# Kernel optimization log

Measured on AMD Instinct MI355X. Metric: run time of the kernel, lower is better.

Reference implementation:

```python
import jax, jax.numpy as jnp
import numpy as np

HEADS = 16
DIM_HEAD = 64
SCALE = DIM_HEAD ** -0.5
EPS = 1e-5


def _bitlinear(x, w):
    """BitNet b1.58 BitLinear (kyegomez/BitNet), eval-mode, bias-free.
    w: [out, in] torch-layout. Ternary weight quant (scale = mean|w|),
    per-token int8 absmax activation quant, straight-through estimator.
    """
    ws = 1.0 / jnp.clip(jnp.mean(jnp.abs(w)), EPS, None)
    wq = jnp.clip(jnp.round(w * ws), -1.0, 1.0) / ws
    wq = w + jax.lax.stop_gradient(wq - w)
    xs = 127.0 / jnp.clip(jnp.max(jnp.abs(x), axis=-1, keepdims=True), EPS, None)
    xq = jnp.clip(jnp.round(x * xs), -128.0, 127.0) / xs
    xq = x + jax.lax.stop_gradient(xq - x)
    return jnp.einsum('bnd,od->bno', xq, wq)


def setup_inputs() -> dict:
    key = jax.random.key(0)
    ks = jax.random.split(key, 6)
    b, n, d = 2, 2048, 1024
    return {
        'x': jax.random.normal(ks[0], (b, n, d), dtype=jnp.float32),
        'context': jax.random.normal(ks[1], (b, n, d), dtype=jnp.float32),
        'Wq': jax.random.normal(ks[2], (d, d), dtype=jnp.float32) * 0.02,
        'Wk': jax.random.normal(ks[3], (d, d), dtype=jnp.float32) * 0.02,
        'Wv': jax.random.normal(ks[4], (d, d), dtype=jnp.float32) * 0.02,
        'Wo': jax.random.normal(ks[5], (d, d), dtype=jnp.float32) * 0.02,
    }


def reference(x, context, Wq, Wk, Wv, Wo):
    b, n, _ = x.shape
    m = context.shape[1]
    q = _bitlinear(x, Wq)
    k = _bitlinear(context, Wk)
    v = _bitlinear(context, Wv)
    # b n (h d) -> b h n d
    q = q.reshape(b, n, HEADS, DIM_HEAD).transpose(0, 2, 1, 3)
    k = k.reshape(b, m, HEADS, DIM_HEAD).transpose(0, 2, 1, 3)
    v = v.reshape(b, m, HEADS, DIM_HEAD).transpose(0, 2, 1, 3)
    dots = jnp.einsum('bhid,bhjd->bhij', q, k) * SCALE
    attn = jax.nn.softmax(dots, axis=-1)  # dropout is identity in eval
    out = jnp.einsum('bhij,bhjd->bhid', attn, v)
    out = out.transpose(0, 2, 1, 3).reshape(b, n, HEADS * DIM_HEAD)
    return _bitlinear(out, Wo)
```

## Files before the change

### kernel.cpp

```cpp
#include <hip/hip_runtime.h>
#include <math.h>

#define HEADS   16
#define DHEAD   64
#define SEQ     2048
#define NB      2
#define DM      1024
#define NTOK    4096
#define WEPS    1e-5

using f16x8   = __attribute__((ext_vector_type(8))) _Float16;
using f16x4   = __attribute__((ext_vector_type(4))) _Float16;
using floatx4 = __attribute__((ext_vector_type(4))) float;
using i32x4   = __attribute__((ext_vector_type(4))) int;

typedef __attribute__((address_space(1))) unsigned int gu32;
typedef __attribute__((address_space(3))) unsigned int lu32;

#define BAR_LGKM()  asm volatile("s_waitcnt lgkmcnt(0)\n\ts_barrier" ::: "memory")
#define WAIT_LGKM() asm volatile("s_waitcnt lgkmcnt(0)" ::: "memory")

__device__ __forceinline__ unsigned pack2(_Float16 a, _Float16 b) {
    union { _Float16 h[2]; unsigned u; } c; c.h[0] = a; c.h[1] = b; return c.u;
}
__device__ __forceinline__ _Float16 lo16(unsigned u) {
    union { unsigned u; _Float16 h[2]; } c; c.u = u; return c.h[0];
}
__device__ __forceinline__ _Float16 hi16(unsigned u) {
    union { unsigned u; _Float16 h[2]; } c; c.u = u; return c.h[1];
}
__device__ __forceinline__ unsigned short h16b(_Float16 h) {
    union { _Float16 h; unsigned short u; } c; c.h = h; return c.u;
}

__global__ void wsum1(const float* __restrict__ w0, const float* __restrict__ w1,
                      const float* __restrict__ w2, const float* __restrict__ w3,
                      double* __restrict__ partial) {
    const float* w = (blockIdx.y == 0) ? w0 : (blockIdx.y == 1) ? w1 : (blockIdx.y == 2) ? w2 : w3;
    int base = blockIdx.x * 16384;
    double s = 0.0;
    for (int i = threadIdx.x; i < 16384; i += 256)
        s += fabs((double)w[base + i]);
    __shared__ double sd[256];
    sd[threadIdx.x] = s;
    __syncthreads();
    for (int st = 128; st > 0; st >>= 1) {
        if (threadIdx.x < st) sd[threadIdx.x] += sd[threadIdx.x + st];
        __syncthreads();
    }
    if (threadIdx.x == 0) partial[blockIdx.y * 64 + blockIdx.x] = sd[0];
}

__global__ void wsum2(const double* __restrict__ partial, double* __restrict__ wscale) {
    int t = threadIdx.x;
    if (t < 4) {
        double s = 0.0;
        for (int i = 0; i < 64; i++) s += partial[t * 64 + i];
        double mean = s / (1024.0 * 1024.0);
        wscale[t] = (mean > WEPS) ? mean : WEPS;
    }
}

__global__ void wquant(const float* __restrict__ w0, const float* __restrict__ w1,
                       const float* __restrict__ w2, const float* __restrict__ w3,
                       const double* __restrict__ wscale, signed char* __restrict__ wq) {
    int widx = blockIdx.y;
    const float* w = (widx == 0) ? w0 : (widx == 1) ? w1 : (widx == 2) ? w2 : w3;
    double ws = 1.0 / wscale[widx];
    int idx = (blockIdx.x * 256 + threadIdx.x) * 4;
    float4 wv = *(const float4*)(w + idx);
    char4 o;
    {
        double r = rint((double)wv.x * ws); r = r > 1.0 ? 1.0 : (r < -1.0 ? -1.0 : r); o.x = (signed char)r;
    } {
        double r = rint((double)wv.y * ws); r = r > 1.0 ? 1.0 : (r < -1.0 ? -1.0 : r); o.y = (signed char)r;
    } {
        double r = rint((double)wv.z * ws); r = r > 1.0 ? 1.0 : (r < -1.0 ? -1.0 : r); o.z = (signed char)r;
    } {
        double r = rint((double)wv.w * ws); r = r > 1.0 ? 1.0 : (r < -1.0 ? -1.0 : r); o.w = (signed char)r;
    }
    *(char4*)(wq + (size_t)widx * 1048576 + idx) = o;
}

__device__ __forceinline__ void aquant_row(const float* __restrict__ row,
                                           signed char* __restrict__ dst_row,
                                           double* __restrict__ ascale_p) {
    int t = threadIdx.x;
    float4 xv = *(const float4*)(row + t * 4);
    float a = fmaxf(fmaxf(fabsf(xv.x), fabsf(xv.y)), fmaxf(fabsf(xv.z), fabsf(xv.w)));
    __shared__ float sm[256];
    sm[t] = a;
    __syncthreads();
    for (int st = 128; st > 0; st >>= 1) {
        if (t < st) sm[t] = fmaxf(sm[t], sm[t + st]);
        __syncthreads();
    }
    double mx = (double)sm[0];
    if (mx < WEPS) mx = WEPS;
    if (t == 0) *ascale_p = mx / 127.0;
    double xs = 127.0 / mx;
    char4 o;
    {
        double r = rint((double)xv.x * xs); r = r > 127.0 ? 127.0 : (r < -128.0 ? -128.0 : r); o.x = (signed char)r;
    } {
        double r = rint((double)xv.y * xs); r = r > 127.0 ? 127.0 : (r < -128.0 ? -128.0 : r); o.y = (signed char)r;
    } {
        double r = rint((double)xv.z * xs); r = r > 127.0 ? 127.0 : (r < -128.0 ? -128.0 : r); o.z = (signed char)r;
    } {
        double r = rint((double)xv.w * xs); r = r > 127.0 ? 127.0 : (r < -128.0 ? -128.0 : r); o.w = (signed char)r;
    }
    *(char4*)(dst_row + t * 4) = o;
}

__global__ void aquant(const float* __restrict__ src, signed char* __restrict__ dst,
                       double* __restrict__ ascale) {
    int tok = blockIdx.x;
    aquant_row(src + (size_t)tok * DM, dst + (size_t)tok * DM, ascale + tok);
}

__global__ void aquant2(const float* __restrict__ x, const float* __restrict__ ctx,
                        signed char* __restrict__ dst, double* __restrict__ ascale) {
    int tok = blockIdx.x;
    const float* row = (tok < NTOK) ? x + (size_t)tok * DM : ctx + (size_t)(tok - NTOK) * DM;
    aquant_row(row, dst + (size_t)tok * DM, ascale + tok);
}

__device__ __forceinline__ void gemm_core(
        const signed char* __restrict__ A, const signed char* __restrict__ W,
        const double* __restrict__ ascale, double wsc,
        void* __restrict__ outp, int mode, float prescale, int bx, int by) {
    __shared__ __align__(16) signed char lds_a[128 * 64];
    __shared__ __align__(16) signed char lds_b[128 * 64];
    const int tid  = threadIdx.x;
    const int wave = tid >> 6, lane = tid & 63;
    const int wr = wave >> 1, wc = wave & 1;
    const int quad = lane >> 4, l15 = lane & 15;
    const int row0 = by * 128, col0 = bx * 128;
    i32x4 acc[4][4] = {};

    const signed char* ga0 = A + (size_t)(row0 + (lane >> 2)) * DM + (lane & 3) * 16;
    const signed char* gb0 = W + (size_t)(col0 + (lane >> 2)) * DM + (lane & 3) * 16;

    for (int k0 = 0; k0 < DM; k0 += 64) {
        __syncthreads();
        #pragma unroll
        for (int t = 0; t < 2; t++) {
            const int i = wave + t * 4;
            __builtin_amdgcn_global_load_lds(
                (const gu32*)(const void*)(ga0 + (size_t)i * 16 * DM + k0),
                (lu32*)(void*)(lds_a + i * 1024), 16, 0, 0);
            __builtin_amdgcn_global_load_lds(
                (const gu32*)(const void*)(gb0 + (size_t)i * 16 * DM + k0),
                (lu32*)(void*)(lds_b + i * 1024), 16, 0, 0);
        }
        __syncthreads();
        i32x4 af[4], bfr[4];
        #pragma unroll
        for (int mi = 0; mi < 4; mi++) {
            int r = wr * 64 + mi * 16 + l15;
            af[mi] = *(const i32x4*)&lds_a[r * 64 + quad * 16];
        }
        #pragma unroll
        for (int ni = 0; ni < 4; ni++) {
            int n = wc * 64 + ni * 16 + l15;
            bfr[ni] = *(const i32x4*)&lds_b[n * 64 + quad * 16];
        }
        #pragma unroll
        for (int mi = 0; mi < 4; mi++)
            #pragma unroll
            for (int ni = 0; ni < 4; ni++)
                acc[mi][ni] = __builtin_amdgcn_mfma_i32_16x16x64_i8(af[mi], bfr[ni], acc[mi][ni], 0, 0, 0);
    }

    #pragma unroll
    for (int mi = 0; mi < 4; mi++) {
        int tbase = row0 + wr * 64 + mi * 16 + quad * 4;
        #pragma unroll
        for (int reg = 0; reg < 4; reg++) {
            int t = tbase + reg;
            double sa = ascale[t] * wsc;
            #pragma unroll
            for (int ni = 0; ni < 4; ni++) {
                int o = col0 + wc * 64 + ni * 16 + l15;
                float val = (float)((double)acc[mi][ni][reg] * sa);
                if (mode == 1) {
                    ((float*)outp)[(size_t)t * DM + o] = val;
                } else {
                    int bb = t >> 11, n = t & 2047, hh = o >> 6, dh = o & 63;
                    float fv = val * prescale;
                    _Float16 hl = (_Float16)fv;
                    _Float16 ml = (_Float16)((fv - (float)hl) * 2048.0f);
                    if (mode == 0) {
                        size_t idx = (((size_t)(bb * HEADS + hh) * SEQ + n) << 6) + dh;
                        ((unsigned short*)outp)[idx]           = h16b(hl);
                        ((unsigned short*)outp)[idx + 4194304] = h16b(ml);
                    } else {
                        ((unsigned*)outp)[(((size_t)(bb * HEADS + hh) * 64 + dh) << 11) + n] = pack2(hl, ml);
                    }
                }
            }
        }
    }
}

__global__ __launch_bounds__(256) void gemm_qkv(
        const signed char* __restrict__ xq, const signed char* __restrict__ cq,
        const signed char* __restrict__ wqb, const double* __restrict__ ascale_x,
        const double* __restrict__ wscale, void* __restrict__ qkv) {
    const int which = blockIdx.x >> 3;
    char* base = (char*)qkv + (size_t)which * 16777216;
    gemm_core(which == 0 ? xq : cq,
              wqb + (size_t)which * 1048576,
              ascale_x + (which ? NTOK : 0),
              wscale[which],
              base,
              which == 2 ? 2 : 0,
              which == 0 ? 0.18033688011112042f : 1.0f, blockIdx.x & 7, blockIdx.y);
}

__global__ __launch_bounds__(256) void gemm_o(
        const signed char* __restrict__ aq, const signed char* __restrict__ wo,
        const double* __restrict__ ascale, const double* __restrict__ wscale_p,
        float* __restrict__ out) {
    gemm_core(aq, wo, ascale, *wscale_p, out, 1, 1.0f, blockIdx.x, blockIdx.y);
}

#define KH_IDX(row, d8) (((row) * 8 + ((d8) ^ ((row) & 7))) * 8)

__global__ __launch_bounds__(256, 2) void attn_mfma(
        const unsigned short* __restrict__ qhg, const unsigned short* __restrict__ qlg,
        const unsigned short* __restrict__ khg, const unsigned short* __restrict__ klg,
        const unsigned* __restrict__ vg, float* __restrict__ out) {
    __shared__ __align__(16) _Float16 KhL[32 * 64];
    __shared__ __align__(16) _Float16 KlL[32 * 64];
    __shared__ __align__(16) _Float16 PhL[4][32 * 36];
    __shared__ __align__(16) _Float16 PlL[4][32 * 36];
    __shared__ float Lp[4][2][16][4];

    const int lin  = blockIdx.x;
    const int bh   = (lin & 7) * 4 + (lin >> 7);
    const int qblk = (lin >> 3) & 15;
    const int tid  = threadIdx.x;
    const int wave = tid >> 6, lane = tid & 63;
    const int l15  = lane & 15, quad = lane >> 4;
    const int qbase = qblk * 128 + wave * 32;

    f16x8 qh[2][2], qm[2][2];
    #pragma unroll
    for (int qs = 0; qs < 2; qs++) {
        #pragma unroll
        for (int c = 0; c < 2; c++) {
            size_t off = (((size_t)bh * SEQ + qbase + qs * 16 + l15) << 6) + c * 32 + quad * 8;
            qh[qs][c] = *(const f16x8*)(qhg + off);
            qm[qs][c] = *(const f16x8*)(qlg + off);
        }
    }

    floatx4 och[2][4] = {};
    floatx4 ocm[2][4] = {};
    float lsum[2] = {0.f, 0.f};

    const unsigned short* khb = khg + ((size_t)bh * SEQ << 6);
    const unsigned short* klb = klg + ((size_t)bh * SEQ << 6);
    const unsigned* vbase = vg + ((size_t)bh << 17);

    const int kk = tid >> 3, d8 = tid & 7;

    uint4 kh_pf = *(const uint4*)(khb + ((size_t)kk << 6) + d8 * 8);
    uint4 kl_pf = *(const uint4*)(klb + ((size_t)kk << 6) + d8 * 8);

    for (int kt = 0; kt < SEQ; kt += 32) {
        uint4 va[4], vb[4];
        #pragma unroll
        for (int nh = 0; nh < 4; nh++) {
            const unsigned* vp = vbase + (((size_t)(nh * 16 + l15)) << 11) + kt + quad * 8;
            va[nh] = *(const uint4*)vp;
            vb[nh] = *(const uint4*)(vp + 4);
        }

        BAR_LGKM();

        *(uint4*)&KhL[KH_IDX(kk, d8)] = kh_pf;
        *(uint4*)&KlL[KH_IDX(kk, d8)] = kl_pf;

        if (kt + 32 < SEQ) {
            kh_pf = *(const uint4*)(khb + ((size_t)(kt + 32 + kk) << 6) + d8 * 8);
            kl_pf = *(const uint4*)(klb + ((size_t)(kt + 32 + kk) << 6) + d8 * 8);
        }

        BAR_LGKM();

        f16x8 kfh[2][2], kfl[2][2];
        #pragma unroll
        for (int ms = 0; ms < 2; ms++) {
            #pragma unroll
            for (int c = 0; c < 2; c++) {
                kfh[ms][c] = *(const f16x8*)&KhL[KH_IDX(ms * 16 + l15, c * 4 + quad)];
                kfl[ms][c] = *(const f16x8*)&KlL[KH_IDX(ms * 16 + l15, c * 4 + quad)];
            }
        }

        #pragma unroll
        for (int qs = 0; qs < 2; qs++) {
            #pragma unroll
            for (int ms = 0; ms < 2; ms++) {
                floatx4 ah = {}, am = {};
                #pragma unroll
                for (int c = 0; c < 2; c++) {
                    ah = __builtin_amdgcn_mfma_f32_16x16x32_f16(kfh[ms][c], qh[qs][c], ah, 0, 0, 0);
                    am = __builtin_amdgcn_mfma_f32_16x16x32_f16(kfh[ms][c], qm[qs][c], am, 0, 0, 0);
                    am = __builtin_amdgcn_mfma_f32_16x16x32_f16(kfl[ms][c], qh[qs][c], am, 0, 0, 0);
                }
                float p[4];
                #pragma unroll
                for (int r = 0; r < 4; r++) {
                    float s = ah[r] + am[r] * 4.8828125e-4f;
                    p[r] = exp2f(s);
                    lsum[qs] += p[r];
                }
                f16x4 hv, lv;
                #pragma unroll
                for (int r = 0; r < 4; r++) {
                    _Float16 h = (_Float16)p[r];
                    hv[r] = h;
                    lv[r] = (_Float16)((p[r] - (float)h) * 2048.0f);
                }
                int poff = (qs * 16 + l15) * 36 + ms * 16 + quad * 4;
                *(f16x4*)&PhL[wave][poff] = hv;
                *(f16x4*)&PlL[wave][poff] = lv;
            }
        }
        WAIT_LGKM();

        f16x8 vfh[4], vfm[4];
        #pragma unroll
        for (int nh = 0; nh < 4; nh++) {
            unsigned wd[8] = {va[nh].x, va[nh].y, va[nh].z, va[nh].w,
                              vb[nh].x, vb[nh].y, vb[nh].z, vb[nh].w};
            #pragma unroll
            for (int j = 0; j < 8; j++) { vfh[nh][j] = lo16(wd[j]); vfm[nh][j] = hi16(wd[j]); }
        }
        #pragma unroll
        for (int qs = 0; qs < 2; qs++) {
            f16x8 pfh = *(const f16x8*)&PhL[wave][(qs * 16 + l15) * 36 + quad * 8];
            f16x8 pfm = *(const f16x8*)&PlL[wave][(qs * 16 + l15) * 36 + quad * 8];
            #pragma unroll
            for (int nh = 0; nh < 4; nh++) {
                och[qs][nh] = __builtin_amdgcn_mfma_f32_16x16x32_f16(pfh, vfh[nh], och[qs][nh], 0, 0, 0);
                ocm[qs][nh] = __builtin_amdgcn_mfma_f32_16x16x32_f16(pfh, vfm[nh], ocm[qs][nh], 0, 0, 0);
                ocm[qs][nh] = __builtin_amdgcn_mfma_f32_16x16x32_f16(pfm, vfh[nh], ocm[qs][nh], 0, 0, 0);
            }
        }
    }

    Lp[wave][0][l15][quad] = lsum[0];
    Lp[wave][1][l15][quad] = lsum[1];
    WAIT_LGKM();

    int b = bh >> 4, h = bh & 15;
    #pragma unroll
    for (int qs = 0; qs < 2; qs++) {
        float linv[4];
        #pragma unroll
        for (int r = 0; r < 4; r++) {
            float4 lv = *(const float4*)&Lp[wave][qs][quad * 4 + r][0];
            linv[r] = 1.0f / (lv.x + lv.y + lv.z + lv.w);
        }
        #pragma unroll
        for (int nh = 0; nh < 4; nh++) {
            #pragma unroll
            for (int r = 0; r < 4; r++) {
                int token = b * SEQ + qbase + qs * 16 + quad * 4 + r;
                float val = (och[qs][nh][r] + ocm[qs][nh][r] * 4.8828125e-4f) * linv[r];
                out[(size_t)token * DM + h * 64 + nh * 16 + l15] = val;
            }
        }
    }
}

extern "C" void kernel_launch(void* const* d_in, const int* in_sizes, int n_in,
                              void* d_out, int out_size, void* d_ws, size_t ws_size,
                              hipStream_t stream) {
    const float* x       = (const float*)d_in[0];
    const float* context = (const float*)d_in[1];
    const float* Wq      = (const float*)d_in[2];
    const float* Wk      = (const float*)d_in[3];
    const float* Wv      = (const float*)d_in[4];
    const float* Wo      = (const float*)d_in[5];
    char* ws = (char*)d_ws;

    double* wscale   = (double*)(ws + 0);
    double* partial  = (double*)(ws + 4096);
    double* ascale_x = (double*)(ws + 8192);
    double* ascale_a = (double*)(ws + 73728);
    signed char* wqb = (signed char*)(ws + 131072);
    signed char* xq  = (signed char*)(ws + 4325376);
    signed char* cq  = (signed char*)(ws + 8519680);
    float* attn_out  = (float*)(ws + 4325376);
    char* planes     = ws + 21102592;
    signed char* aq  = (signed char*)(ws + 21102592);

    unsigned short* qhg = (unsigned short*)planes;
    unsigned short* qlg = qhg + 4194304;
    unsigned short* khg = (unsigned short*)(planes + 16777216);
    unsigned short* klg = khg + 4194304;
    unsigned*       vpg = (unsigned*)(planes + 33554432);

    wsum1<<<dim3(64, 4), 256, 0, stream>>>(Wq, Wk, Wv, Wo, partial);
    wsum2<<<1, 64, 0, stream>>>(partial, wscale);
    wquant<<<dim3(1024, 4), 256, 0, stream>>>(Wq, Wk, Wv, Wo, wscale, wqb);
    aquant2<<<2 * NTOK, 256, 0, stream>>>(x, context, xq, ascale_x);

    gemm_qkv<<<dim3(24, 32), 256, 0, stream>>>(xq, cq, wqb, ascale_x, wscale, planes);

    attn_mfma<<<dim3(512), 256, 0, stream>>>(qhg, qlg, khg, klg, vpg, attn_out);

    aquant<<<NTOK, 256, 0, stream>>>(attn_out, aq, ascale_a);
    gemm_o<<<dim3(8, 32), 256, 0, stream>>>(aq, wqb + 3145728, ascale_a, wscale + 3, (float*)d_out);
}
```

Measured before the change: 300.2 us.

## Stage V tiles in shared memory and halve per-block query tile in attention

The attention kernel now gives each wave 16 query rows instead of 32 and launches twice as many blocks, targeting higher occupancy (launch bounds raised to 4 blocks). V tiles are no longer loaded straight from global memory into registers by every wave. They are now cooperatively prefetched, split into high and low fp16 planes, and stored in swizzled shared memory that all waves read from. This is meant to cut redundant global V traffic and register pressure. The cost is more K/V tile loading per query row, since each block now covers fewer queries, plus extra LDS writes and reads.

```diff
diff --git a/kernel.cpp b/kernel.cpp
--- a/kernel.cpp
+++ b/kernel.cpp
@@ -227,65 +227,79 @@
 
 #define KH_IDX(row, d8) (((row) * 8 + ((d8) ^ ((row) & 7))) * 8)
 
-__global__ __launch_bounds__(256, 2) void attn_mfma(
+__global__ __launch_bounds__(256, 4) void attn_mfma(
         const unsigned short* __restrict__ qhg, const unsigned short* __restrict__ qlg,
         const unsigned short* __restrict__ khg, const unsigned short* __restrict__ klg,
         const unsigned* __restrict__ vg, float* __restrict__ out) {
     __shared__ __align__(16) _Float16 KhL[32 * 64];
     __shared__ __align__(16) _Float16 KlL[32 * 64];
-    __shared__ __align__(16) _Float16 PhL[4][32 * 36];
-    __shared__ __align__(16) _Float16 PlL[4][32 * 36];
-    __shared__ float Lp[4][2][16][4];
+    __shared__ __align__(16) _Float16 VhL[64 * 32];
+    __shared__ __align__(16) _Float16 VlL[64 * 32];
+    __shared__ __align__(16) _Float16 PhL[4][16 * 36];
+    __shared__ __align__(16) _Float16 PlL[4][16 * 36];
+    __shared__ float Lp[4][16][4];
 
     const int lin  = blockIdx.x;
-    const int bh   = (lin & 7) * 4 + (lin >> 7);
-    const int qblk = (lin >> 3) & 15;
+    const int bh   = (lin & 7) * 4 + (lin >> 8);
+    const int qblk = (lin >> 3) & 31;
     const int tid  = threadIdx.x;
     const int wave = tid >> 6, lane = tid & 63;
     const int l15  = lane & 15, quad = lane >> 4;
-    const int qbase = qblk * 128 + wave * 32;
-
-    f16x8 qh[2][2], qm[2][2];
+    const int qbase = qblk * 64 + wave * 16;
+
+    f16x8 qh[2], qm[2];
     #pragma unroll
-    for (int qs = 0; qs < 2; qs++) {
-        #pragma unroll
-        for (int c = 0; c < 2; c++) {
-            size_t off = (((size_t)bh * SEQ + qbase + qs * 16 + l15) << 6) + c * 32 + quad * 8;
-            qh[qs][c] = *(const f16x8*)(qhg + off);
-            qm[qs][c] = *(const f16x8*)(qlg + off);
-        }
-    }
-
-    floatx4 och[2][4] = {};
-    floatx4 ocm[2][4] = {};
-    float lsum[2] = {0.f, 0.f};
+    for (int c = 0; c < 2; c++) {
+        size_t off = (((size_t)bh * SEQ + qbase + l15) << 6) + c * 32 + quad * 8;
+        qh[c] = *(const f16x8*)(qhg + off);
+        qm[c] = *(const f16x8*)(qlg + off);
+    }
+
+    floatx4 och[4] = {};
+    floatx4 ocm[4] = {};
+    float lsum = 0.f;
 
     const unsigned short* khb = khg + ((size_t)bh * SEQ << 6);
     const unsigned short* klb = klg + ((size_t)bh * SEQ << 6);
     const unsigned* vbase = vg + ((size_t)bh << 17);
 
     const int kk = tid >> 3, d8 = tid & 7;
+    const int vrow = tid >> 2, vc = tid & 3;
+    const int vcs  = vc ^ (vrow & 3);
+    const unsigned* vsrc = vbase + ((size_t)vrow << 11) + vc * 8;
 
     uint4 kh_pf = *(const uint4*)(khb + ((size_t)kk << 6) + d8 * 8);
     uint4 kl_pf = *(const uint4*)(klb + ((size_t)kk << 6) + d8 * 8);
+    uint4 vp0 = *(const uint4*)(vsrc);
+    uint4 vp1 = *(const uint4*)(vsrc + 4);
 
     for (int kt = 0; kt < SEQ; kt += 32) {
-        uint4 va[4], vb[4];
-        #pragma unroll
-        for (int nh = 0; nh < 4; nh++) {
-            const unsigned* vp = vbase + (((size_t)(nh * 16 + l15)) << 11) + kt + quad * 8;
-            va[nh] = *(const uint4*)vp;
-            vb[nh] = *(const uint4*)(vp + 4);
-        }
-
         BAR_LGKM();
 
         *(uint4*)&KhL[KH_IDX(kk, d8)] = kh_pf;
         *(uint4*)&KlL[KH_IDX(kk, d8)] = kl_pf;
+
+        uint4 vh4, vl4;
+        {
+            unsigned w0 = vp0.x, w1 = vp0.y, w2 = vp0.z, w3 = vp0.w;
+            vh4.x = (w0 & 0xffffu) | (w1 << 16);
+            vl4.x = (w0 >> 16)     | (w1 & 0xffff0000u);
+            vh4.y = (w2 & 0xffffu) | (w3 << 16);
+            vl4.y = (w2 >> 16)     | (w3 & 0xffff0000u);
+            w0 = vp1.x; w1 = vp1.y; w2 = vp1.z; w3 = vp1.w;
+            vh4.z = (w0 & 0xffffu) | (w1 << 16);
+            vl4.z = (w0 >> 16)     | (w1 & 0xffff0000u);
+            vh4.w = (w0 = vp1.z, (w0 & 0xffffu)) | (vp1.w << 16);
+            vl4.w = (vp1.z >> 16)  | (vp1.w & 0xffff0000u);
+        }
+        *(uint4*)&VhL[(vrow * 4 + vcs) * 8] = vh4;
+        *(uint4*)&VlL[(vrow * 4 + vcs) * 8] = vl4;
 
         if (kt + 32 < SEQ) {
             kh_pf = *(const uint4*)(khb + ((size_t)(kt + 32 + kk) << 6) + d8 * 8);
             kl_pf = *(const uint4*)(klb + ((size_t)(kt + 32 + kk) << 6) + d8 * 8);
+            vp0 = *(const uint4*)(vsrc + kt + 32);
+            vp1 = *(const uint4*)(vsrc + kt + 36);
         }
 
         BAR_LGKM();
@@ -301,79 +315,65 @@
         }
 
         #pragma unroll
-        for (int qs = 0; qs < 2; qs++) {
-            #pragma unroll
-            for (int ms = 0; ms < 2; ms++) {
-                floatx4 ah = {}, am = {};
-                #pragma unroll
-                for (int c = 0; c < 2; c++) {
-                    ah = __builtin_amdgcn_mfma_f32_16x16x32_f16(kfh[ms][c], qh[qs][c], ah, 0, 0, 0);
-                    am = __builtin_amdgcn_mfma_f32_16x16x32_f16(kfh[ms][c], qm[qs][c], am, 0, 0, 0);
-                    am = __builtin_amdgcn_mfma_f32_16x16x32_f16(kfl[ms][c], qh[qs][c], am, 0, 0, 0);
-                }
-                float p[4];
-                #pragma unroll
-                for (int r = 0; r < 4; r++) {
-                    float s = ah[r] + am[r] * 4.8828125e-4f;
-                    p[r] = exp2f(s);
-                    lsum[qs] += p[r];
-                }
-                f16x4 hv, lv;
-                #pragma unroll
-                for (int r = 0; r < 4; r++) {
-                    _Float16 h = (_Float16)p[r];
-                    hv[r] = h;
-                    lv[r] = (_Float16)((p[r] - (float)h) * 2048.0f);
-                }
-                int poff = (qs * 16 + l15) * 36 + ms * 16 + quad * 4;
-                *(f16x4*)&PhL[wave][poff] = hv;
-                *(f16x4*)&PlL[wave][poff] = lv;
+        for (int ms = 0; ms < 2; ms++) {
+            floatx4 ah = {}, am = {};
+            #pragma unroll
+            for (int c = 0; c < 2; c++) {
+                ah = __builtin_amdgcn_mfma_f32_16x16x32_f16(kfh[ms][c], qh[c], ah, 0, 0, 0);
+                am = __builtin_amdgcn_mfma_f32_16x16x32_f16(kfh[ms][c], qm[c], am, 0, 0, 0);
+                am = __builtin_amdgcn_mfma_f32_16x16x32_f16(kfl[ms][c], qh[c], am, 0, 0, 0);
             }
+            float p[4];
+            #pragma unroll
+            for (int r = 0; r < 4; r++) {
+                float s = ah[r] + am[r] * 4.8828125e-4f;
+                p[r] = exp2f(s);
+                lsum += p[r];
+            }
+            f16x4 hv, lv;
+            #pragma unroll
+            for (int r = 0; r < 4; r++) {
+                _Float16 h = (_Float16)p[r];
+                hv[r] = h;
+                lv[r] = (_Float16)((p[r] - (float)h) * 2048.0f);
+            }
+            int poff = l15 * 36 + ms * 16 + quad * 4;
+            *(f16x4*)&PhL[wave][poff] = hv;
+            *(f16x4*)&PlL[wave][poff] = lv;
         }
         WAIT_LGKM();
 
-        f16x8 vfh[4], vfm[4];
+        f16x8 pfh = *(const f16x8*)&PhL[wave][l15 * 36 + quad * 8];
+        f16x8 pfm = *(const f16x8*)&PlL[wave][l15 * 36 + quad * 8];
         #pragma unroll
         for (int nh = 0; nh < 4; nh++) {
-            unsigned wd[8] = {va[nh].x, va[nh].y, va[nh].z, va[nh].w,
-                              vb[nh].x, vb[nh].y, vb[nh].z, vb[nh].w};
-            #pragma unroll
-            for (int j = 0; j < 8; j++) { vfh[nh][j] = lo16(wd[j]); vfm[nh][j] = hi16(wd[j]); }
-        }
-        #pragma unroll
-        for (int qs = 0; qs < 2; qs++) {
-            f16x8 pfh = *(const f16x8*)&PhL[wave][(qs * 16 + l15) * 36 + quad * 8];
-            f16x8 pfm = *(const f16x8*)&PlL[wave][(qs * 16 + l15) * 36 + quad * 8];
-            #pragma unroll
-            for (int nh = 0; nh < 4; nh++) {
-                och[qs][nh] = __builtin_amdgcn_mfma_f32_16x16x32_f16(pfh, vfh[nh], och[qs][nh], 0, 0, 0);
-                ocm[qs][nh] = __builtin_amdgcn_mfma_f32_16x16x32_f16(pfh, vfm[nh], ocm[qs][nh], 0, 0, 0);
-                ocm[qs][nh] = __builtin_amdgcn_mfma_f32_16x16x32_f16(pfm, vfh[nh], ocm[qs][nh], 0, 0, 0);
-            }
-        }
-    }
-
-    Lp[wave][0][l15][quad] = lsum[0];
-    Lp[wave][1][l15][quad] = lsum[1];
+            int vro = nh * 16 + l15;
+            int vof = (vro * 4 + (quad ^ (vro & 3))) * 8;
+            f16x8 vfh = *(const f16x8*)&VhL[vof];
+            f16x8 vfm = *(const f16x8*)&VlL[vof];
+            och[nh] = __builtin_amdgcn_mfma_f32_16x16x32_f16(pfh, vfh, och[nh], 0, 0, 0);
+            ocm[nh] = __builtin_amdgcn_mfma_f32_16x16x32_f16(pfh, vfm, ocm[nh], 0, 0, 0);
+            ocm[nh] = __builtin_amdgcn_mfma_f32_16x16x32_f16(pfm, vfh, ocm[nh], 0, 0, 0);
+        }
+    }
+
+    Lp[wave][l15][quad] = lsum;
     WAIT_LGKM();
 
     int b = bh >> 4, h = bh & 15;
+    float linv[4];
     #pragma unroll
-    for (int qs = 0; qs < 2; qs++) {
-        float linv[4];
+    for (int r = 0; r < 4; r++) {
+        float4 lv = *(const float4*)&Lp[wave][quad * 4 + r][0];
+        linv[r] = 1.0f / (lv.x + lv.y + lv.z + lv.w);
+    }
+    #pragma unroll
+    for (int nh = 0; nh < 4; nh++) {
         #pragma unroll
         for (int r = 0; r < 4; r++) {
-            float4 lv = *(const float4*)&Lp[wave][qs][quad * 4 + r][0];
-            linv[r] = 1.0f / (lv.x + lv.y + lv.z + lv.w);
-        }
-        #pragma unroll
-        for (int nh = 0; nh < 4; nh++) {
-            #pragma unroll
-            for (int r = 0; r < 4; r++) {
-                int token = b * SEQ + qbase + qs * 16 + quad * 4 + r;
-                float val = (och[qs][nh][r] + ocm[qs][nh][r] * 4.8828125e-4f) * linv[r];
-                out[(size_t)token * DM + h * 64 + nh * 16 + l15] = val;
-            }
+            int token = b * SEQ + qbase + quad * 4 + r;
+            float val = (och[nh][r] + ocm[nh][r] * 4.8828125e-4f) * linv[r];
+            out[(size_t)token * DM + h * 64 + nh * 16 + l15] = val;
         }
     }
 }
@@ -413,7 +413,7 @@
 
     gemm_qkv<<<dim3(24, 32), 256, 0, stream>>>(xq, cq, wqb, ascale_x, wscale, planes);
 
-    attn_mfma<<<dim3(512), 256, 0, stream>>>(qhg, qlg, khg, klg, vpg, attn_out);
+    attn_mfma<<<dim3(1024), 256, 0, stream>>>(qhg, qlg, khg, klg, vpg, attn_out);
 
     aquant<<<NTOK, 256, 0, stream>>>(attn_out, aq, ascale_a);
     gemm_o<<<dim3(8, 32), 256, 0, stream>>>(aq, wqb + 3145728, ascale_a, wscale + 3, (float*)d_out);
```

New measurement: 304.4 us. About the same (+1.4%).

## Tile V into separate hi/lo planes per 32-key block and restructure attention loop

Applied to the files above, without the earlier changes.

The V projection epilogue now writes separate fp16 hi and lo planes in a tiled [bh][key tile][dh][32] layout with vectorized 4-element stores, replacing the packed interleaved u32 layout. This lets the attention kernel load V fragments directly without unpacking, and it prefetches the next tile's V after the PV MFMAs. The attention loop also separates the QK MFMAs from the softmax, wraps the MFMA sections in s_setprio, uses hardware exp2 and packed RTZ conversion, and remaps the block-to-(bh, qblk) ordering. RTZ conversion changes rounding slightly, and register pressure rises from holding the prefetched V fragments.

```diff
diff --git a/kernel.cpp b/kernel.cpp
--- a/kernel.cpp
+++ b/kernel.cpp
@@ -11,6 +11,7 @@
 
 using f16x8   = __attribute__((ext_vector_type(8))) _Float16;
 using f16x4   = __attribute__((ext_vector_type(4))) _Float16;
+using fp16x2  = __attribute__((ext_vector_type(2))) __fp16;
 using floatx4 = __attribute__((ext_vector_type(4))) float;
 using i32x4   = __attribute__((ext_vector_type(4))) int;
 
@@ -20,17 +21,11 @@
 #define BAR_LGKM()  asm volatile("s_waitcnt lgkmcnt(0)\n\ts_barrier" ::: "memory")
 #define WAIT_LGKM() asm volatile("s_waitcnt lgkmcnt(0)" ::: "memory")
 
-__device__ __forceinline__ unsigned pack2(_Float16 a, _Float16 b) {
-    union { _Float16 h[2]; unsigned u; } c; c.h[0] = a; c.h[1] = b; return c.u;
-}
-__device__ __forceinline__ _Float16 lo16(unsigned u) {
-    union { unsigned u; _Float16 h[2]; } c; c.u = u; return c.h[0];
-}
-__device__ __forceinline__ _Float16 hi16(unsigned u) {
-    union { unsigned u; _Float16 h[2]; } c; c.u = u; return c.h[1];
-}
 __device__ __forceinline__ unsigned short h16b(_Float16 h) {
     union { _Float16 h; unsigned short u; } c; c.h = h; return c.u;
+}
+__device__ __forceinline__ unsigned pk2u(fp16x2 v) {
+    union { fp16x2 h; unsigned u; } c; c.h = v; return c.u;
 }
 
 __global__ void wsum1(const float* __restrict__ w0, const float* __restrict__ w1,
@@ -175,27 +170,46 @@
     #pragma unroll
     for (int mi = 0; mi < 4; mi++) {
         int tbase = row0 + wr * 64 + mi * 16 + quad * 4;
-        #pragma unroll
-        for (int reg = 0; reg < 4; reg++) {
-            int t = tbase + reg;
-            double sa = ascale[t] * wsc;
+        if (mode == 2) {
+            int bb = tbase >> 11, n = tbase & 2047;
+            int tile = n >> 5, tin = n & 31;
             #pragma unroll
             for (int ni = 0; ni < 4; ni++) {
                 int o = col0 + wc * 64 + ni * 16 + l15;
-                float val = (float)((double)acc[mi][ni][reg] * sa);
-                if (mode == 1) {
-                    ((float*)outp)[(size_t)t * DM + o] = val;
-                } else {
-                    int bb = t >> 11, n = t & 2047, hh = o >> 6, dh = o & 63;
-                    float fv = val * prescale;
+                int hh = o >> 6, dh = o & 63;
+                ushort4 hv, lv;
+                #pragma unroll
+                for (int reg = 0; reg < 4; reg++) {
+                    double sa = ascale[tbase + reg] * wsc;
+                    float fv = (float)((double)acc[mi][ni][reg] * sa) * prescale;
                     _Float16 hl = (_Float16)fv;
                     _Float16 ml = (_Float16)((fv - (float)hl) * 2048.0f);
-                    if (mode == 0) {
+                    ((unsigned short*)&hv)[reg] = h16b(hl);
+                    ((unsigned short*)&lv)[reg] = h16b(ml);
+                }
+                size_t idx = (((size_t)(bb * HEADS + hh) * 64 + tile) * 64 + dh) * 32 + tin;
+                *(ushort4*)((unsigned short*)outp + idx)           = hv;
+                *(ushort4*)((unsigned short*)outp + idx + 4194304) = lv;
+            }
+        } else {
+            #pragma unroll
+            for (int reg = 0; reg < 4; reg++) {
+                int t = tbase + reg;
+                double sa = ascale[t] * wsc;
+                #pragma unroll
+                for (int ni = 0; ni < 4; ni++) {
+                    int o = col0 + wc * 64 + ni * 16 + l15;
+                    float val = (float)((double)acc[mi][ni][reg] * sa);
+                    if (mode == 1) {
+                        ((float*)outp)[(size_t)t * DM + o] = val;
+                    } else {
+                        int bb = t >> 11, n = t & 2047, hh = o >> 6, dh = o & 63;
+                        float fv = val * prescale;
+                        _Float16 hl = (_Float16)fv;
+                        _Float16 ml = (_Float16)((fv - (float)hl) * 2048.0f);
                         size_t idx = (((size_t)(bb * HEADS + hh) * SEQ + n) << 6) + dh;
                         ((unsigned short*)outp)[idx]           = h16b(hl);
                         ((unsigned short*)outp)[idx + 4194304] = h16b(ml);
-                    } else {
-                        ((unsigned*)outp)[(((size_t)(bb * HEADS + hh) * 64 + dh) << 11) + n] = pack2(hl, ml);
                     }
                 }
             }
@@ -230,7 +244,8 @@
 __global__ __launch_bounds__(256, 2) void attn_mfma(
         const unsigned short* __restrict__ qhg, const unsigned short* __restrict__ qlg,
         const unsigned short* __restrict__ khg, const unsigned short* __restrict__ klg,
-        const unsigned* __restrict__ vg, float* __restrict__ out) {
+        const unsigned short* __restrict__ vhg, const unsigned short* __restrict__ vlg,
+        float* __restrict__ out) {
     __shared__ __align__(16) _Float16 KhL[32 * 64];
     __shared__ __align__(16) _Float16 KlL[32 * 64];
     __shared__ __align__(16) _Float16 PhL[4][32 * 36];
@@ -238,8 +253,8 @@
     __shared__ float Lp[4][2][16][4];
 
     const int lin  = blockIdx.x;
-    const int bh   = (lin & 7) * 4 + (lin >> 7);
-    const int qblk = (lin >> 3) & 15;
+    const int bh   = (lin & 7) * 4 + ((lin >> 3) & 3);
+    const int qblk = lin >> 5;
     const int tid  = threadIdx.x;
     const int wave = tid >> 6, lane = tid & 63;
     const int l15  = lane & 15, quad = lane >> 4;
@@ -259,33 +274,34 @@
     floatx4 och[2][4] = {};
     floatx4 ocm[2][4] = {};
     float lsum[2] = {0.f, 0.f};
+    const floatx4 zf = {};
 
     const unsigned short* khb = khg + ((size_t)bh * SEQ << 6);
     const unsigned short* klb = klg + ((size_t)bh * SEQ << 6);
-    const unsigned* vbase = vg + ((size_t)bh << 17);
+    const unsigned short* vhb = vhg + ((size_t)bh << 17);
+    const unsigned short* vlb = vlg + ((size_t)bh << 17);
 
     const int kk = tid >> 3, d8 = tid & 7;
 
     uint4 kh_pf = *(const uint4*)(khb + ((size_t)kk << 6) + d8 * 8);
     uint4 kl_pf = *(const uint4*)(klb + ((size_t)kk << 6) + d8 * 8);
-
-    for (int kt = 0; kt < SEQ; kt += 32) {
-        uint4 va[4], vb[4];
-        #pragma unroll
-        for (int nh = 0; nh < 4; nh++) {
-            const unsigned* vp = vbase + (((size_t)(nh * 16 + l15)) << 11) + kt + quad * 8;
-            va[nh] = *(const uint4*)vp;
-            vb[nh] = *(const uint4*)(vp + 4);
-        }
-
+    f16x8 vfh[4], vfm[4];
+    #pragma unroll
+    for (int nh = 0; nh < 4; nh++) {
+        size_t vo = ((size_t)(nh * 16 + l15) << 5) + quad * 8;
+        vfh[nh] = *(const f16x8*)(vhb + vo);
+        vfm[nh] = *(const f16x8*)(vlb + vo);
+    }
+
+    for (int t = 0; t < 64; t++) {
         BAR_LGKM();
 
         *(uint4*)&KhL[KH_IDX(kk, d8)] = kh_pf;
         *(uint4*)&KlL[KH_IDX(kk, d8)] = kl_pf;
 
-        if (kt + 32 < SEQ) {
-            kh_pf = *(const uint4*)(khb + ((size_t)(kt + 32 + kk) << 6) + d8 * 8);
-            kl_pf = *(const uint4*)(klb + ((size_t)(kt + 32 + kk) << 6) + d8 * 8);
+        if (t + 1 < 64) {
+            kh_pf = *(const uint4*)(khb + ((size_t)((t + 1) * 32 + kk) << 6) + d8 * 8);
+            kl_pf = *(const uint4*)(klb + ((size_t)((t + 1) * 32 + kk) << 6) + d8 * 8);
         }
 
         BAR_LGKM();
@@ -300,46 +316,45 @@
             }
         }
 
+        __builtin_amdgcn_s_setprio(1);
+        floatx4 ah[2][2], am[2][2];
         #pragma unroll
         for (int qs = 0; qs < 2; qs++) {
             #pragma unroll
             for (int ms = 0; ms < 2; ms++) {
-                floatx4 ah = {}, am = {};
-                #pragma unroll
-                for (int c = 0; c < 2; c++) {
-                    ah = __builtin_amdgcn_mfma_f32_16x16x32_f16(kfh[ms][c], qh[qs][c], ah, 0, 0, 0);
-                    am = __builtin_amdgcn_mfma_f32_16x16x32_f16(kfh[ms][c], qm[qs][c], am, 0, 0, 0);
-                    am = __builtin_amdgcn_mfma_f32_16x16x32_f16(kfl[ms][c], qh[qs][c], am, 0, 0, 0);
-                }
-                float p[4];
-                #pragma unroll
-                for (int r = 0; r < 4; r++) {
-                    float s = ah[r] + am[r] * 4.8828125e-4f;
-                    p[r] = exp2f(s);
-                    lsum[qs] += p[r];
-                }
-                f16x4 hv, lv;
-                #pragma unroll
-                for (int r = 0; r < 4; r++) {
-                    _Float16 h = (_Float16)p[r];
-                    hv[r] = h;
-                    lv[r] = (_Float16)((p[r] - (float)h) * 2048.0f);
-                }
+                ah[qs][ms] = __builtin_amdgcn_mfma_f32_16x16x32_f16(kfh[ms][0], qh[qs][0], zf, 0, 0, 0);
+                am[qs][ms] = __builtin_amdgcn_mfma_f32_16x16x32_f16(kfh[ms][0], qm[qs][0], zf, 0, 0, 0);
+                am[qs][ms] = __builtin_amdgcn_mfma_f32_16x16x32_f16(kfl[ms][0], qh[qs][0], am[qs][ms], 0, 0, 0);
+                ah[qs][ms] = __builtin_amdgcn_mfma_f32_16x16x32_f16(kfh[ms][1], qh[qs][1], ah[qs][ms], 0, 0, 0);
+                am[qs][ms] = __builtin_amdgcn_mfma_f32_16x16x32_f16(kfh[ms][1], qm[qs][1], am[qs][ms], 0, 0, 0);
+                am[qs][ms] = __builtin_amdgcn_mfma_f32_16x16x32_f16(kfl[ms][1], qh[qs][1], am[qs][ms], 0, 0, 0);
+            }
+        }
+        __builtin_amdgcn_s_setprio(0);
+
+        #pragma unroll
+        for (int qs = 0; qs < 2; qs++) {
+            #pragma unroll
+            for (int ms = 0; ms < 2; ms++) {
+                float p0 = __builtin_amdgcn_exp2f(ah[qs][ms][0] + am[qs][ms][0] * 4.8828125e-4f);
+                float p1 = __builtin_amdgcn_exp2f(ah[qs][ms][1] + am[qs][ms][1] * 4.8828125e-4f);
+                float p2 = __builtin_amdgcn_exp2f(ah[qs][ms][2] + am[qs][ms][2] * 4.8828125e-4f);
+                float p3 = __builtin_amdgcn_exp2f(ah[qs][ms][3] + am[qs][ms][3] * 4.8828125e-4f);
+                lsum[qs] += (p0 + p1) + (p2 + p3);
+                fp16x2 h01 = __builtin_amdgcn_cvt_pkrtz(p0, p1);
+                fp16x2 h23 = __builtin_amdgcn_cvt_pkrtz(p2, p3);
+                fp16x2 m01 = __builtin_amdgcn_cvt_pkrtz((p0 - (float)h01[0]) * 2048.0f,
+                                                        (p1 - (float)h01[1]) * 2048.0f);
+                fp16x2 m23 = __builtin_amdgcn_cvt_pkrtz((p2 - (float)h23[0]) * 2048.0f,
+                                                        (p3 - (float)h23[1]) * 2048.0f);
                 int poff = (qs * 16 + l15) * 36 + ms * 16 + quad * 4;
-                *(f16x4*)&PhL[wave][poff] = hv;
-                *(f16x4*)&PlL[wave][poff] = lv;
+                *(uint2*)&PhL[wave][poff] = make_uint2(pk2u(h01), pk2u(h23));
+                *(uint2*)&PlL[wave][poff] = make_uint2(pk2u(m01), pk2u(m23));
             }
         }
         WAIT_LGKM();
 
-        f16x8 vfh[4], vfm[4];
-        #pragma unroll
-        for (int nh = 0; nh < 4; nh++) {
-            unsigned wd[8] = {va[nh].x, va[nh].y, va[nh].z, va[nh].w,
-                              vb[nh].x, vb[nh].y, vb[nh].z, vb[nh].w};
-            #pragma unroll
-            for (int j = 0; j < 8; j++) { vfh[nh][j] = lo16(wd[j]); vfm[nh][j] = hi16(wd[j]); }
-        }
+        __builtin_amdgcn_s_setprio(1);
         #pragma unroll
         for (int qs = 0; qs < 2; qs++) {
             f16x8 pfh = *(const f16x8*)&PhL[wave][(qs * 16 + l15) * 36 + quad * 8];
@@ -349,6 +364,16 @@
                 och[qs][nh] = __builtin_amdgcn_mfma_f32_16x16x32_f16(pfh, vfh[nh], och[qs][nh], 0, 0, 0);
                 ocm[qs][nh] = __builtin_amdgcn_mfma_f32_16x16x32_f16(pfh, vfm[nh], ocm[qs][nh], 0, 0, 0);
                 ocm[qs][nh] = __builtin_amdgcn_mfma_f32_16x16x32_f16(pfm, vfh[nh], ocm[qs][nh], 0, 0, 0);
+            }
+        }
+        __builtin_amdgcn_s_setprio(0);
+
+        if (t + 1 < 64) {
+            #pragma unroll
+            for (int nh = 0; nh < 4; nh++) {
+                size_t vo = ((size_t)((t + 1) * 64 + nh * 16 + l15) << 5) + quad * 8;
+                vfh[nh] = *(const f16x8*)(vhb + vo);
+                vfm[nh] = *(const f16x8*)(vlb + vo);
             }
         }
     }
@@ -404,7 +429,8 @@
     unsigned short* qlg = qhg + 4194304;
     unsigned short* khg = (unsigned short*)(planes + 16777216);
     unsigned short* klg = khg + 4194304;
-    unsigned*       vpg = (unsigned*)(planes + 33554432);
+    unsigned short* vhg = (unsigned short*)(planes + 33554432);
+    unsigned short* vlg = vhg + 4194304;
 
     wsum1<<<dim3(64, 4), 256, 0, stream>>>(Wq, Wk, Wv, Wo, partial);
     wsum2<<<1, 64, 0, stream>>>(partial, wscale);
@@ -413,7 +439,7 @@
 
     gemm_qkv<<<dim3(24, 32), 256, 0, stream>>>(xq, cq, wqb, ascale_x, wscale, planes);
 
-    attn_mfma<<<dim3(512), 256, 0, stream>>>(qhg, qlg, khg, klg, vpg, attn_out);
+    attn_mfma<<<dim3(512), 256, 0, stream>>>(qhg, qlg, khg, klg, vhg, vlg, attn_out);
 
     aquant<<<NTOK, 256, 0, stream>>>(attn_out, aq, ascale_a);
     gemm_o<<<dim3(8, 32), 256, 0, stream>>>(aq, wqb + 3145728, ascale_a, wscale + 3, (float*)d_out);
```

Result: faster. 269.8 us (-10.1%).
